# Kernel optimization log

Hardware: AMD Instinct MI355X
Metric: run time of the kernel (lower is better)

Reference implementation:

```python
import jax, jax.numpy as jnp
import numpy as np
import math

N_NODES = 50000
N_EDGES = 1600000
DIM = 64
HEADS = 8
EDGE_DIM = 32


def setup_inputs() -> dict:
    key = jax.random.key(0)
    ks = jax.random.split(key, 12)
    s = 1.0 / math.sqrt(DIM)
    se = 1.0 / math.sqrt(EDGE_DIM)
    return {
        'x': jax.random.normal(ks[0], (N_NODES, DIM), jnp.float32),
        'edge_index': jax.random.randint(ks[1], (2, N_EDGES), 0, N_NODES),
        'edge_attr': jax.random.normal(ks[2], (N_EDGES, EDGE_DIM), jnp.float32),
        'WQ': jax.random.normal(ks[3], (DIM, DIM), jnp.float32) * s,
        'bQ': jnp.zeros((DIM,), jnp.float32),
        'WK': jax.random.normal(ks[4], (DIM, DIM), jnp.float32) * s,
        'bK': jnp.zeros((DIM,), jnp.float32),
        'WV': jax.random.normal(ks[5], (DIM, DIM), jnp.float32) * s,
        'bV': jnp.zeros((DIM,), jnp.float32),
        'WO': jax.random.normal(ks[6], (DIM, DIM), jnp.float32) * s,
        'bO': jnp.zeros((DIM,), jnp.float32),
        'We1': jax.random.normal(ks[7], (EDGE_DIM, EDGE_DIM), jnp.float32) * se,
        'be1': jnp.zeros((EDGE_DIM,), jnp.float32),
        'We2': jax.random.normal(ks[8], (EDGE_DIM, HEADS), jnp.float32) * se,
        'be2': jnp.zeros((HEADS,), jnp.float32),
    }


def graph_softmax(src, index, num_segments):
    # src: [E, H], index: [E] -> per-destination-node stable softmax
    smax = jax.ops.segment_max(src, index, num_segments=num_segments)  # [N, H]
    smax = jnp.where(jnp.isfinite(smax), smax, 0.0)  # nodes with no edges
    e = jnp.exp(src - smax[index])
    ssum = jax.ops.segment_sum(e, index, num_segments=num_segments) + 1e-12
    return e / ssum[index]


def reference(x, edge_index, edge_attr, WQ, bQ, WK, bK, WV, bV, WO, bO, We1, be1, We2, be2):
    num_nodes = x.shape[0]
    d_k = DIM // HEADS
    i, j = edge_index[0], edge_index[1]
    # per-node projections [N, H, d_k], then gather per-edge
    Q = (x @ WQ + bQ).reshape(num_nodes, HEADS, d_k)
    K = (x @ WK + bK).reshape(num_nodes, HEADS, d_k)
    V = (x @ WV + bV).reshape(num_nodes, HEADS, d_k)
    query = Q[j]  # [E, H, d_k]
    key = K[i]
    value = V[i]
    # edge bias MLP: [edge_dim -> edge_dim -> num_heads] with SiLU between
    h = jax.nn.silu(edge_attr @ We1 + be1)
    bias = h @ We2 + be2  # [E, H]
    scores = jnp.sum(query * key, axis=-1) / math.sqrt(d_k) + bias  # [E, H]
    alpha = graph_softmax(scores, j, num_nodes)  # [E, H]
    weighted = (alpha[..., None] * value).reshape(-1, DIM)  # [E, dim]
    attn_out = jax.ops.segment_sum(weighted, j, num_segments=num_nodes)  # [N, dim]
    return attn_out @ WO + bO
```

## Files before the change

### kernel.cpp

```cpp
#include <hip/hip_runtime.h>
#include <math.h>

#define N_NODES 50000
#define N_EDGES 1600000
#define DIM 64
#define HEADS 8
#define EDGE_DIM 32

#define NB 256
#define NPB 196
#define ACAP 8192
#define PART_T 512
#define EPT 4
#define PART_E (PART_T * EPT)

typedef __fp16 h2 __attribute__((ext_vector_type(2)));

__device__ __forceinline__ unsigned int f2bf(float f) {
    union { float f; unsigned int u; } c; c.f = f;
    unsigned int u = c.u;
    return (u + 0x7FFFu + ((u >> 16) & 1u)) >> 16;
}
__device__ __forceinline__ float bf_lo(unsigned int u) { return __uint_as_float(u << 16); }
__device__ __forceinline__ float bf_hi(unsigned int u) { return __uint_as_float(u & 0xFFFF0000u); }

__global__ __launch_bounds__(1024) void pack_weights(
    const float* __restrict__ We1, const float* __restrict__ We2,
    h2* __restrict__ w1p, h2* __restrict__ w2p)
{
    const int t = threadIdx.x;
    if (t < 512) {
        const int c = t >> 4, kk = t & 15;
        w1p[t] = __builtin_amdgcn_cvt_pkrtz(We1[(2 * kk) * EDGE_DIM + c],
                                            We1[(2 * kk + 1) * EDGE_DIM + c]);
    } else if (t < 512 + 128) {
        const int u = t - 512;
        const int h = u >> 4, cc = u & 15;
        w2p[u] = __builtin_amdgcn_cvt_pkrtz(We2[(2 * cc) * HEADS + h],
                                            We2[(2 * cc + 1) * HEADS + h]);
    }
}

__global__ __launch_bounds__(512) void mlp_partition(
    const int* __restrict__ ei,
    const float* __restrict__ edge_attr,
    const h2* __restrict__ w1p, const float* __restrict__ be1,
    const h2* __restrict__ w2p, const float* __restrict__ be2,
    int* __restrict__ gcur,
    unsigned int* __restrict__ A_rec, uint4* __restrict__ A_bias)
{
    __shared__ int cnt[NB];
    __shared__ int base[NB];
    __shared__ int lbase[NB];
    __shared__ int total_s;
    __shared__ unsigned int srec[PART_E];
    __shared__ uint4 sbias[PART_E];
    __shared__ unsigned char sbkt[PART_E];
    const int tid = threadIdx.x;
    if (tid < NB) cnt[tid] = 0;
    __syncthreads();
    const int e0 = blockIdx.x * PART_E;
    #pragma unroll
    for (int k = 0; k < EPT; ++k) {
        const int e = e0 + k * PART_T + tid;
        if (e < N_EDGES) atomicAdd(&cnt[ei[N_EDGES + e] / NPB], 1);
    }
    __syncthreads();
    if (tid < NB) lbase[tid] = cnt[tid];
    __syncthreads();
    for (int o = 1; o < NB; o <<= 1) {
        int t = 0;
        if (tid < NB && tid >= o) t = lbase[tid - o];
        __syncthreads();
        if (tid < NB) lbase[tid] += t;
        __syncthreads();
    }
    if (tid < NB) {
        const int inc = lbase[tid];
        const int c = cnt[tid];
        base[tid] = (c > 0) ? atomicAdd(&gcur[tid], c) : 0;
        lbase[tid] = inc - c;
        if (tid == NB - 1) total_s = inc;
        cnt[tid] = 0;
    }
    __syncthreads();
    for (int k = 0; k < EPT; ++k) {
        const int e = e0 + k * PART_T + tid;
        if (e >= N_EDGES) break;
        const int i = ei[e];
        const int j = ei[N_EDGES + e];
        const int b = j / NPB;
        const int jl = j - b * NPB;
        float a[EDGE_DIM];
        const float4* ar = (const float4*)(edge_attr + (size_t)e * EDGE_DIM);
        #pragma unroll
        for (int q = 0; q < EDGE_DIM / 4; ++q) {
            float4 v = ar[q];
            a[q * 4 + 0] = v.x; a[q * 4 + 1] = v.y;
            a[q * 4 + 2] = v.z; a[q * 4 + 3] = v.w;
        }
        h2 a2[EDGE_DIM / 2];
        #pragma unroll
        for (int kk = 0; kk < EDGE_DIM / 2; ++kk)
            a2[kk] = __builtin_amdgcn_cvt_pkrtz(a[2 * kk], a[2 * kk + 1]);
        float sil[EDGE_DIM];
        #pragma unroll 8
        for (int c = 0; c < EDGE_DIM; ++c) {
            float s = be1[c];
            #pragma unroll
            for (int kk = 0; kk < EDGE_DIM / 2; ++kk)
                s = __builtin_amdgcn_fdot2(a2[kk], w1p[c * 16 + kk], s, false);
            sil[c] = __fdividef(s, 1.0f + __expf(-s));
        }
        h2 s2[EDGE_DIM / 2];
        #pragma unroll
        for (int cc = 0; cc < EDGE_DIM / 2; ++cc)
            s2[cc] = __builtin_amdgcn_cvt_pkrtz(sil[2 * cc], sil[2 * cc + 1]);
        float b0f = be2[0], b1f = be2[1], b2f = be2[2], b3f = be2[3];
        float b4f = be2[4], b5f = be2[5], b6f = be2[6], b7f = be2[7];
        #pragma unroll
        for (int cc = 0; cc < EDGE_DIM / 2; ++cc) {
            b0f = __builtin_amdgcn_fdot2(s2[cc], w2p[0 * 16 + cc], b0f, false);
            b1f = __builtin_amdgcn_fdot2(s2[cc], w2p[1 * 16 + cc], b1f, false);
            b2f = __builtin_amdgcn_fdot2(s2[cc], w2p[2 * 16 + cc], b2f, false);
            b3f = __builtin_amdgcn_fdot2(s2[cc], w2p[3 * 16 + cc], b3f, false);
            b4f = __builtin_amdgcn_fdot2(s2[cc], w2p[4 * 16 + cc], b4f, false);
            b5f = __builtin_amdgcn_fdot2(s2[cc], w2p[5 * 16 + cc], b5f, false);
            b6f = __builtin_amdgcn_fdot2(s2[cc], w2p[6 * 16 + cc], b6f, false);
            b7f = __builtin_amdgcn_fdot2(s2[cc], w2p[7 * 16 + cc], b7f, false);
        }
        uint4 br;
        br.x = f2bf(b0f) | (f2bf(b1f) << 16);
        br.y = f2bf(b2f) | (f2bf(b3f) << 16);
        br.z = f2bf(b4f) | (f2bf(b5f) << 16);
        br.w = f2bf(b6f) | (f2bf(b7f) << 16);
        const int s = lbase[b] + atomicAdd(&cnt[b], 1);
        srec[s] = ((unsigned)jl << 24) | (unsigned)i;
        sbias[s] = br;
        sbkt[s] = (unsigned char)b;
    }
    __syncthreads();
    const int total = total_s;
    for (int s = tid; s < total; s += PART_T) {
        const int b = sbkt[s];
        const int gp = base[b] + (s - lbase[b]);
        if (gp < ACAP) {
            A_rec[(size_t)b * ACAP + gp]  = srec[s];
            A_bias[(size_t)b * ACAP + gp] = sbias[s];
        }
    }
}

__global__ __launch_bounds__(512) void bucket_perm(
    const int* __restrict__ gcur,
    const unsigned int* __restrict__ A_rec,
    int* __restrict__ offs, int* __restrict__ src_sorted, int* __restrict__ perm)
{
    __shared__ int sc[NB];
    __shared__ int ldeg[NPB];
    __shared__ int loff[NPB + 1];
    __shared__ int gbase_s;
    const int tid = threadIdx.x;
    const int b = blockIdx.x;
    if (tid < NB) sc[tid] = min(gcur[tid], ACAP);
    __syncthreads();
    for (int o = 1; o < NB; o <<= 1) {
        int t = 0;
        if (tid < NB && tid >= o) t = sc[tid - o];
        __syncthreads();
        if (tid < NB) sc[tid] += t;
        __syncthreads();
    }
    if (tid == 0) gbase_s = (b == 0) ? 0 : sc[b - 1];
    if (tid < NPB) ldeg[tid] = 0;
    __syncthreads();
    const int gbase = gbase_s;
    const int nb = min(gcur[b], ACAP);
    for (int r = tid; r < nb; r += 512)
        atomicAdd(&ldeg[A_rec[(size_t)b * ACAP + r] >> 24], 1);
    __syncthreads();
    if (tid < 256) sc[tid] = (tid < NPB) ? ldeg[tid] : 0;
    __syncthreads();
    for (int o = 1; o < 256; o <<= 1) {
        int t = 0;
        if (tid < 256 && tid >= o) t = sc[tid - o];
        __syncthreads();
        if (tid < 256) sc[tid] += t;
        __syncthreads();
    }
    if (tid == 0) loff[0] = 0;
    if (tid < NPB) { loff[tid + 1] = sc[tid]; ldeg[tid] = 0; }
    __syncthreads();
    const int jbase = b * NPB;
    if (tid < NPB && jbase + tid < N_NODES) offs[jbase + tid] = gbase + loff[tid];
    if (b == NB - 1 && tid == 0) offs[N_NODES] = gbase + nb;
    for (int r = tid; r < nb; r += 512) {
        const unsigned int rec = A_rec[(size_t)b * ACAP + r];
        const int jl = rec >> 24;
        const int slot = loff[jl] + atomicAdd(&ldeg[jl], 1);
        const int gp = gbase + slot;
        src_sorted[gp] = (int)(rec & 0xFFFFFFu);
        perm[gp] = b * ACAP + r;
    }
}

__global__ __launch_bounds__(256) void qkv_proj(
    const float* __restrict__ x,
    const float* __restrict__ WQ, const float* __restrict__ bQ,
    const float* __restrict__ WK, const float* __restrict__ bK,
    const float* __restrict__ WV, const float* __restrict__ bV,
    float* __restrict__ Q, unsigned int* __restrict__ KV)
{
    __shared__ float sWQ[DIM * DIM];
    __shared__ float sWK[DIM * DIM];
    __shared__ float sWV[DIM * DIM];
    for (int t = threadIdx.x; t < DIM * DIM; t += blockDim.x) {
        sWQ[t] = WQ[t]; sWK[t] = WK[t]; sWV[t] = WV[t];
    }
    __syncthreads();
    const int lane = threadIdx.x & 63;
    const int wave = threadIdx.x >> 6;
    const int n = blockIdx.x * 4 + wave;
    if (n >= N_NODES) return;
    float xl = x[(size_t)n * DIM + lane];
    float aq = bQ[lane], ak = bK[lane], av = bV[lane];
    #pragma unroll
    for (int k = 0; k < DIM; ++k) {
        float xv = __shfl(xl, k, 64);
        aq += xv * sWQ[k * DIM + lane];
        ak += xv * sWK[k * DIM + lane];
        av += xv * sWV[k * DIM + lane];
    }
    Q[(size_t)n * DIM + lane] = aq;
    KV[(size_t)n * DIM + lane] = f2bf(ak) | (f2bf(av) << 16);
}

__global__ __launch_bounds__(256) void node_attn_out(
    const int* __restrict__ off,
    const int* __restrict__ src_sorted,
    const int* __restrict__ perm,
    const unsigned short* __restrict__ bias_u16,
    const float* __restrict__ Q, const unsigned int* __restrict__ KV,
    const float* __restrict__ WO, const float* __restrict__ bO,
    float* __restrict__ out)
{
    __shared__ float sWO[DIM * DIM];
    for (int t = threadIdx.x; t < DIM * DIM; t += 256) sWO[t] = WO[t];
    __syncthreads();
    const int lane = threadIdx.x & 63;
    const int wave = threadIdx.x >> 6;
    const int j = blockIdx.x * 4 + wave;
    if (j >= N_NODES) return;
    const int beg = off[j], end = off[j + 1];
    const int h = lane >> 3;
    const float qv = Q[(size_t)j * DIM + lane];
    const float inv_sqrt_dk = 0.35355339059327373f;
    float num = 0.0f;
    float den = 1e-12f;
    int t = beg;
    for (; t + 3 < end; t += 4) {
        const int i0 = src_sorted[t + 0];
        const int i1 = src_sorted[t + 1];
        const int i2 = src_sorted[t + 2];
        const int i3 = src_sorted[t + 3];
        const int p0 = perm[t + 0];
        const int p1 = perm[t + 1];
        const int p2 = perm[t + 2];
        const int p3 = perm[t + 3];
        const unsigned int u0 = KV[(size_t)i0 * DIM + lane];
        const unsigned int u1 = KV[(size_t)i1 * DIM + lane];
        const unsigned int u2 = KV[(size_t)i2 * DIM + lane];
        const unsigned int u3 = KV[(size_t)i3 * DIM + lane];
        const float b0 = bf_lo((unsigned int)bias_u16[(size_t)p0 * HEADS + h]);
        const float b1 = bf_lo((unsigned int)bias_u16[(size_t)p1 * HEADS + h]);
        const float b2 = bf_lo((unsigned int)bias_u16[(size_t)p2 * HEADS + h]);
        const float b3 = bf_lo((unsigned int)bias_u16[(size_t)p3 * HEADS + h]);
        float d0 = qv * bf_lo(u0);
        float d1 = qv * bf_lo(u1);
        float d2 = qv * bf_lo(u2);
        float d3 = qv * bf_lo(u3);
        d0 += __shfl_xor(d0, 1, 64); d1 += __shfl_xor(d1, 1, 64);
        d2 += __shfl_xor(d2, 1, 64); d3 += __shfl_xor(d3, 1, 64);
        d0 += __shfl_xor(d0, 2, 64); d1 += __shfl_xor(d1, 2, 64);
        d2 += __shfl_xor(d2, 2, 64); d3 += __shfl_xor(d3, 2, 64);
        d0 += __shfl_xor(d0, 4, 64); d1 += __shfl_xor(d1, 4, 64);
        d2 += __shfl_xor(d2, 4, 64); d3 += __shfl_xor(d3, 4, 64);
        const float e0 = __expf(d0 * inv_sqrt_dk + b0);
        const float e1 = __expf(d1 * inv_sqrt_dk + b1);
        const float e2 = __expf(d2 * inv_sqrt_dk + b2);
        const float e3 = __expf(d3 * inv_sqrt_dk + b3);
        num += e0 * bf_hi(u0) + e1 * bf_hi(u1) + e2 * bf_hi(u2) + e3 * bf_hi(u3);
        den += e0 + e1 + e2 + e3;
    }
    for (; t < end; ++t) {
        const int i0 = src_sorted[t];
        const unsigned int u0 = KV[(size_t)i0 * DIM + lane];
        const float b0 = bf_lo((unsigned int)bias_u16[(size_t)perm[t] * HEADS + h]);
        float d0 = qv * bf_lo(u0);
        d0 += __shfl_xor(d0, 1, 64);
        d0 += __shfl_xor(d0, 2, 64);
        d0 += __shfl_xor(d0, 4, 64);
        const float e0 = __expf(d0 * inv_sqrt_dk + b0);
        num += e0 * bf_hi(u0);
        den += e0;
    }
    const float av = num / den;
    float acc = bO[lane];
    #pragma unroll
    for (int k = 0; k < DIM; ++k) {
        acc += __shfl(av, k, 64) * sWO[k * DIM + lane];
    }
    out[(size_t)j * DIM + lane] = acc;
}

extern "C" void kernel_launch(void* const* d_in, const int* in_sizes, int n_in,
                              void* d_out, int out_size, void* d_ws, size_t ws_size,
                              hipStream_t stream) {
    const float* x    = (const float*)d_in[0];
    const int*   ei   = (const int*)d_in[1];
    const float* ea   = (const float*)d_in[2];
    const float* WQ   = (const float*)d_in[3];
    const float* bQ   = (const float*)d_in[4];
    const float* WK   = (const float*)d_in[5];
    const float* bK   = (const float*)d_in[6];
    const float* WV   = (const float*)d_in[7];
    const float* bV   = (const float*)d_in[8];
    const float* WO   = (const float*)d_in[9];
    const float* bO   = (const float*)d_in[10];
    const float* We1  = (const float*)d_in[11];
    const float* be1  = (const float*)d_in[12];
    const float* We2  = (const float*)d_in[13];
    const float* be2  = (const float*)d_in[14];
    float* out = (float*)d_out;

    char* ws = (char*)d_ws;
    size_t off_b = 0;
    auto alloc = [&](size_t bytes) {
        void* p = ws + off_b;
        off_b += (bytes + 255) & ~(size_t)255;
        return p;
    };
    float*        Q          = (float*)alloc((size_t)N_NODES * DIM * sizeof(float));
    unsigned int* KV         = (unsigned int*)alloc((size_t)N_NODES * DIM * sizeof(unsigned int));
    unsigned int* A_rec      = (unsigned int*)alloc((size_t)NB * ACAP * sizeof(unsigned int));
    uint4*        A_bias     = (uint4*)alloc((size_t)NB * ACAP * sizeof(uint4));
    int*          src_sorted = (int*)alloc((size_t)N_EDGES * sizeof(int));
    int*          perm       = (int*)alloc((size_t)N_EDGES * sizeof(int));
    int*          offs       = (int*)alloc((size_t)(N_NODES + 1) * sizeof(int));
    int*          gcur       = (int*)alloc((size_t)NB * sizeof(int));
    h2*           w1p        = (h2*)alloc(512 * sizeof(h2));
    h2*           w2p        = (h2*)alloc(128 * sizeof(h2));

    (void)hipMemsetAsync(gcur, 0, (size_t)NB * sizeof(int), stream);

    pack_weights<<<1, 1024, 0, stream>>>(We1, We2, w1p, w2p);
    mlp_partition<<<(N_EDGES + PART_E - 1) / PART_E, PART_T, 0, stream>>>(
        ei, ea, w1p, be1, w2p, be2, gcur, A_rec, A_bias);
    bucket_perm<<<NB, 512, 0, stream>>>(gcur, A_rec, offs, src_sorted, perm);
    qkv_proj<<<(N_NODES + 3) / 4, 256, 0, stream>>>(x, WQ, bQ, WK, bK, WV, bV, Q, KV);
    node_attn_out<<<(N_NODES + 3) / 4, 256, 0, stream>>>(offs, src_sorted, perm,
                                                         (const unsigned short*)A_bias,
                                                         Q, KV, WO, bO, out);
}
```

Before: 349.8 us.

## Fuse edge-bias MLP and per-node sorting into the attention kernel

The edge MLP moves out of the partition kernel into a new fused attention kernel, and the separate bucket_perm pass is dropped. Each of 8 blocks per bucket rescans the bucket's records, counting-sorts its 25 destination nodes in LDS, computes the edge biases into shared memory, then runs the per-node softmax aggregation and output projection. This removes the global write and read of per-edge biases and the src_sorted/perm arrays, plus one launch. In exchange, every sub-block rereads the whole bucket, edge_attr is gathered in random order rather than streamed, WO is read from global memory rather than LDS, and edges beyond CAPQ per sub-bucket would be silently dropped.

```diff
diff --git a/kernel.cpp b/kernel.cpp
--- a/kernel.cpp
+++ b/kernel.cpp
@@ -10,8 +10,12 @@
 #define NB 256
 #define NPB 196
 #define ACAP 8192
+#define QS 8
+#define NQ 25
+#define CAPQ 1280
+
 #define PART_T 512
-#define EPT 4
+#define EPT 8
 #define PART_E (PART_T * EPT)
 
 typedef __fp16 h2 __attribute__((ext_vector_type(2)));
@@ -41,20 +45,14 @@
     }
 }
 
-__global__ __launch_bounds__(512) void mlp_partition(
-    const int* __restrict__ ei,
-    const float* __restrict__ edge_attr,
-    const h2* __restrict__ w1p, const float* __restrict__ be1,
-    const h2* __restrict__ w2p, const float* __restrict__ be2,
-    int* __restrict__ gcur,
-    unsigned int* __restrict__ A_rec, uint4* __restrict__ A_bias)
+__global__ __launch_bounds__(512) void partition(
+    const int* __restrict__ ei, int* __restrict__ gcur, uint2* __restrict__ A_rec)
 {
     __shared__ int cnt[NB];
     __shared__ int base[NB];
     __shared__ int lbase[NB];
     __shared__ int total_s;
-    __shared__ unsigned int srec[PART_E];
-    __shared__ uint4 sbias[PART_E];
+    __shared__ uint2 srec[PART_E];
     __shared__ unsigned char sbkt[PART_E];
     const int tid = threadIdx.x;
     if (tid < NB) cnt[tid] = 0;
@@ -84,123 +82,25 @@
         cnt[tid] = 0;
     }
     __syncthreads();
+    #pragma unroll
     for (int k = 0; k < EPT; ++k) {
         const int e = e0 + k * PART_T + tid;
-        if (e >= N_EDGES) break;
-        const int i = ei[e];
-        const int j = ei[N_EDGES + e];
-        const int b = j / NPB;
-        const int jl = j - b * NPB;
-        float a[EDGE_DIM];
-        const float4* ar = (const float4*)(edge_attr + (size_t)e * EDGE_DIM);
-        #pragma unroll
-        for (int q = 0; q < EDGE_DIM / 4; ++q) {
-            float4 v = ar[q];
-            a[q * 4 + 0] = v.x; a[q * 4 + 1] = v.y;
-            a[q * 4 + 2] = v.z; a[q * 4 + 3] = v.w;
-        }
-        h2 a2[EDGE_DIM / 2];
-        #pragma unroll
-        for (int kk = 0; kk < EDGE_DIM / 2; ++kk)
-            a2[kk] = __builtin_amdgcn_cvt_pkrtz(a[2 * kk], a[2 * kk + 1]);
-        float sil[EDGE_DIM];
-        #pragma unroll 8
-        for (int c = 0; c < EDGE_DIM; ++c) {
-            float s = be1[c];
-            #pragma unroll
-            for (int kk = 0; kk < EDGE_DIM / 2; ++kk)
-                s = __builtin_amdgcn_fdot2(a2[kk], w1p[c * 16 + kk], s, false);
-            sil[c] = __fdividef(s, 1.0f + __expf(-s));
-        }
-        h2 s2[EDGE_DIM / 2];
-        #pragma unroll
-        for (int cc = 0; cc < EDGE_DIM / 2; ++cc)
-            s2[cc] = __builtin_amdgcn_cvt_pkrtz(sil[2 * cc], sil[2 * cc + 1]);
-        float b0f = be2[0], b1f = be2[1], b2f = be2[2], b3f = be2[3];
-        float b4f = be2[4], b5f = be2[5], b6f = be2[6], b7f = be2[7];
-        #pragma unroll
-        for (int cc = 0; cc < EDGE_DIM / 2; ++cc) {
-            b0f = __builtin_amdgcn_fdot2(s2[cc], w2p[0 * 16 + cc], b0f, false);
-            b1f = __builtin_amdgcn_fdot2(s2[cc], w2p[1 * 16 + cc], b1f, false);
-            b2f = __builtin_amdgcn_fdot2(s2[cc], w2p[2 * 16 + cc], b2f, false);
-            b3f = __builtin_amdgcn_fdot2(s2[cc], w2p[3 * 16 + cc], b3f, false);
-            b4f = __builtin_amdgcn_fdot2(s2[cc], w2p[4 * 16 + cc], b4f, false);
-            b5f = __builtin_amdgcn_fdot2(s2[cc], w2p[5 * 16 + cc], b5f, false);
-            b6f = __builtin_amdgcn_fdot2(s2[cc], w2p[6 * 16 + cc], b6f, false);
-            b7f = __builtin_amdgcn_fdot2(s2[cc], w2p[7 * 16 + cc], b7f, false);
-        }
-        uint4 br;
-        br.x = f2bf(b0f) | (f2bf(b1f) << 16);
-        br.y = f2bf(b2f) | (f2bf(b3f) << 16);
-        br.z = f2bf(b4f) | (f2bf(b5f) << 16);
-        br.w = f2bf(b6f) | (f2bf(b7f) << 16);
-        const int s = lbase[b] + atomicAdd(&cnt[b], 1);
-        srec[s] = ((unsigned)jl << 24) | (unsigned)i;
-        sbias[s] = br;
-        sbkt[s] = (unsigned char)b;
+        if (e < N_EDGES) {
+            const int i = ei[e];
+            const int j = ei[N_EDGES + e];
+            const int b = j / NPB;
+            const int jl = j - b * NPB;
+            const int s = lbase[b] + atomicAdd(&cnt[b], 1);
+            srec[s] = make_uint2((unsigned)e, ((unsigned)jl << 24) | (unsigned)i);
+            sbkt[s] = (unsigned char)b;
+        }
     }
     __syncthreads();
     const int total = total_s;
     for (int s = tid; s < total; s += PART_T) {
         const int b = sbkt[s];
         const int gp = base[b] + (s - lbase[b]);
-        if (gp < ACAP) {
-            A_rec[(size_t)b * ACAP + gp]  = srec[s];
-            A_bias[(size_t)b * ACAP + gp] = sbias[s];
-        }
-    }
-}
-
-__global__ __launch_bounds__(512) void bucket_perm(
-    const int* __restrict__ gcur,
-    const unsigned int* __restrict__ A_rec,
-    int* __restrict__ offs, int* __restrict__ src_sorted, int* __restrict__ perm)
-{
-    __shared__ int sc[NB];
-    __shared__ int ldeg[NPB];
-    __shared__ int loff[NPB + 1];
-    __shared__ int gbase_s;
-    const int tid = threadIdx.x;
-    const int b = blockIdx.x;
-    if (tid < NB) sc[tid] = min(gcur[tid], ACAP);
-    __syncthreads();
-    for (int o = 1; o < NB; o <<= 1) {
-        int t = 0;
-        if (tid < NB && tid >= o) t = sc[tid - o];
-        __syncthreads();
-        if (tid < NB) sc[tid] += t;
-        __syncthreads();
-    }
-    if (tid == 0) gbase_s = (b == 0) ? 0 : sc[b - 1];
-    if (tid < NPB) ldeg[tid] = 0;
-    __syncthreads();
-    const int gbase = gbase_s;
-    const int nb = min(gcur[b], ACAP);
-    for (int r = tid; r < nb; r += 512)
-        atomicAdd(&ldeg[A_rec[(size_t)b * ACAP + r] >> 24], 1);
-    __syncthreads();
-    if (tid < 256) sc[tid] = (tid < NPB) ? ldeg[tid] : 0;
-    __syncthreads();
-    for (int o = 1; o < 256; o <<= 1) {
-        int t = 0;
-        if (tid < 256 && tid >= o) t = sc[tid - o];
-        __syncthreads();
-        if (tid < 256) sc[tid] += t;
-        __syncthreads();
-    }
-    if (tid == 0) loff[0] = 0;
-    if (tid < NPB) { loff[tid + 1] = sc[tid]; ldeg[tid] = 0; }
-    __syncthreads();
-    const int jbase = b * NPB;
-    if (tid < NPB && jbase + tid < N_NODES) offs[jbase + tid] = gbase + loff[tid];
-    if (b == NB - 1 && tid == 0) offs[N_NODES] = gbase + nb;
-    for (int r = tid; r < nb; r += 512) {
-        const unsigned int rec = A_rec[(size_t)b * ACAP + r];
-        const int jl = rec >> 24;
-        const int slot = loff[jl] + atomicAdd(&ldeg[jl], 1);
-        const int gp = gbase + slot;
-        src_sorted[gp] = (int)(rec & 0xFFFFFFu);
-        perm[gp] = b * ACAP + r;
+        if (gp < ACAP) A_rec[(size_t)b * ACAP + gp] = srec[s];
     }
 }
 
@@ -235,82 +135,170 @@
     KV[(size_t)n * DIM + lane] = f2bf(ak) | (f2bf(av) << 16);
 }
 
-__global__ __launch_bounds__(256) void node_attn_out(
-    const int* __restrict__ off,
-    const int* __restrict__ src_sorted,
-    const int* __restrict__ perm,
-    const unsigned short* __restrict__ bias_u16,
+__global__ __launch_bounds__(256) void attn_fused(
+    const int* __restrict__ gcur, const uint2* __restrict__ A_rec,
+    const float* __restrict__ edge_attr,
+    const h2* __restrict__ w1p, const float* __restrict__ be1,
+    const h2* __restrict__ w2p, const float* __restrict__ be2,
     const float* __restrict__ Q, const unsigned int* __restrict__ KV,
     const float* __restrict__ WO, const float* __restrict__ bO,
     float* __restrict__ out)
 {
-    __shared__ float sWO[DIM * DIM];
-    for (int t = threadIdx.x; t < DIM * DIM; t += 256) sWO[t] = WO[t];
-    __syncthreads();
-    const int lane = threadIdx.x & 63;
-    const int wave = threadIdx.x >> 6;
-    const int j = blockIdx.x * 4 + wave;
-    if (j >= N_NODES) return;
-    const int beg = off[j], end = off[j + 1];
+    __shared__ unsigned int lds_e[CAPQ];
+    __shared__ unsigned short lds_i[CAPQ];
+    __shared__ uint4 sbias[CAPQ];
+    __shared__ int loff[NQ + 1];
+    __shared__ int lcur[NQ];
+    __shared__ int ldeg[NQ];
+    const int tid = threadIdx.x;
+    const int bq = blockIdx.x;
+    const int b = bq >> 3;
+    const int q = bq & 7;
+    const int jl0 = q * NQ;
+    const int jl1 = (jl0 + NQ < NPB) ? jl0 + NQ : NPB;
+    const int nqn = jl1 - jl0;
+    const int nb = min(gcur[b], ACAP);
+    if (tid < NQ) ldeg[tid] = 0;
+    __syncthreads();
+    for (int r = tid; r < nb; r += 256) {
+        const int jl = (int)(A_rec[(size_t)b * ACAP + r].y >> 24);
+        if (jl >= jl0 && jl < jl1) atomicAdd(&ldeg[jl - jl0], 1);
+    }
+    __syncthreads();
+    if (tid < 64) {
+        int v = (tid < nqn) ? ldeg[tid] : 0;
+        #pragma unroll
+        for (int o = 1; o < 32; o <<= 1) {
+            int t = __shfl_up(v, o, 64);
+            if (tid >= o) v += t;
+        }
+        if (tid == 0) loff[0] = 0;
+        if (tid < nqn) { loff[tid + 1] = v; lcur[tid] = 0; }
+    }
+    __syncthreads();
+    for (int r = tid; r < nb; r += 256) {
+        const uint2 rec = A_rec[(size_t)b * ACAP + r];
+        const int jl = (int)(rec.y >> 24);
+        if (jl >= jl0 && jl < jl1) {
+            const int s = loff[jl - jl0] + atomicAdd(&lcur[jl - jl0], 1);
+            if (s < CAPQ) {
+                lds_e[s] = rec.x;
+                lds_i[s] = (unsigned short)(rec.y & 0xFFFFFFu);
+            }
+        }
+    }
+    __syncthreads();
+    const int tot = (loff[nqn] < CAPQ) ? loff[nqn] : CAPQ;
+    for (int s = tid; s < tot; s += 256) {
+        const int e = (int)lds_e[s];
+        float a[EDGE_DIM];
+        const float4* ar = (const float4*)(edge_attr + (size_t)e * EDGE_DIM);
+        #pragma unroll
+        for (int p = 0; p < EDGE_DIM / 4; ++p) {
+            float4 v = ar[p];
+            a[p * 4 + 0] = v.x; a[p * 4 + 1] = v.y;
+            a[p * 4 + 2] = v.z; a[p * 4 + 3] = v.w;
+        }
+        h2 a2[EDGE_DIM / 2];
+        #pragma unroll
+        for (int kk = 0; kk < EDGE_DIM / 2; ++kk)
+            a2[kk] = __builtin_amdgcn_cvt_pkrtz(a[2 * kk], a[2 * kk + 1]);
+        float sil[EDGE_DIM];
+        #pragma unroll 8
+        for (int c = 0; c < EDGE_DIM; ++c) {
+            float sv = be1[c];
+            #pragma unroll
+            for (int kk = 0; kk < EDGE_DIM / 2; ++kk)
+                sv = __builtin_amdgcn_fdot2(a2[kk], w1p[c * 16 + kk], sv, false);
+            sil[c] = __fdividef(sv, 1.0f + __expf(-sv));
+        }
+        h2 s2[EDGE_DIM / 2];
+        #pragma unroll
+        for (int cc = 0; cc < EDGE_DIM / 2; ++cc)
+            s2[cc] = __builtin_amdgcn_cvt_pkrtz(sil[2 * cc], sil[2 * cc + 1]);
+        float b0f = be2[0], b1f = be2[1], b2f = be2[2], b3f = be2[3];
+        float b4f = be2[4], b5f = be2[5], b6f = be2[6], b7f = be2[7];
+        #pragma unroll
+        for (int cc = 0; cc < EDGE_DIM / 2; ++cc) {
+            b0f = __builtin_amdgcn_fdot2(s2[cc], w2p[0 * 16 + cc], b0f, false);
+            b1f = __builtin_amdgcn_fdot2(s2[cc], w2p[1 * 16 + cc], b1f, false);
+            b2f = __builtin_amdgcn_fdot2(s2[cc], w2p[2 * 16 + cc], b2f, false);
+            b3f = __builtin_amdgcn_fdot2(s2[cc], w2p[3 * 16 + cc], b3f, false);
+            b4f = __builtin_amdgcn_fdot2(s2[cc], w2p[4 * 16 + cc], b4f, false);
+            b5f = __builtin_amdgcn_fdot2(s2[cc], w2p[5 * 16 + cc], b5f, false);
+            b6f = __builtin_amdgcn_fdot2(s2[cc], w2p[6 * 16 + cc], b6f, false);
+            b7f = __builtin_amdgcn_fdot2(s2[cc], w2p[7 * 16 + cc], b7f, false);
+        }
+        uint4 br;
+        br.x = f2bf(b0f) | (f2bf(b1f) << 16);
+        br.y = f2bf(b2f) | (f2bf(b3f) << 16);
+        br.z = f2bf(b4f) | (f2bf(b5f) << 16);
+        br.w = f2bf(b6f) | (f2bf(b7f) << 16);
+        sbias[s] = br;
+    }
+    __syncthreads();
+    const int lane = tid & 63;
+    const int wave = tid >> 6;
     const int h = lane >> 3;
-    const float qv = Q[(size_t)j * DIM + lane];
+    const unsigned short* sb16 = (const unsigned short*)sbias;
     const float inv_sqrt_dk = 0.35355339059327373f;
-    float num = 0.0f;
-    float den = 1e-12f;
-    int t = beg;
-    for (; t + 3 < end; t += 4) {
-        const int i0 = src_sorted[t + 0];
-        const int i1 = src_sorted[t + 1];
-        const int i2 = src_sorted[t + 2];
-        const int i3 = src_sorted[t + 3];
-        const int p0 = perm[t + 0];
-        const int p1 = perm[t + 1];
-        const int p2 = perm[t + 2];
-        const int p3 = perm[t + 3];
-        const unsigned int u0 = KV[(size_t)i0 * DIM + lane];
-        const unsigned int u1 = KV[(size_t)i1 * DIM + lane];
-        const unsigned int u2 = KV[(size_t)i2 * DIM + lane];
-        const unsigned int u3 = KV[(size_t)i3 * DIM + lane];
-        const float b0 = bf_lo((unsigned int)bias_u16[(size_t)p0 * HEADS + h]);
-        const float b1 = bf_lo((unsigned int)bias_u16[(size_t)p1 * HEADS + h]);
-        const float b2 = bf_lo((unsigned int)bias_u16[(size_t)p2 * HEADS + h]);
-        const float b3 = bf_lo((unsigned int)bias_u16[(size_t)p3 * HEADS + h]);
-        float d0 = qv * bf_lo(u0);
-        float d1 = qv * bf_lo(u1);
-        float d2 = qv * bf_lo(u2);
-        float d3 = qv * bf_lo(u3);
-        d0 += __shfl_xor(d0, 1, 64); d1 += __shfl_xor(d1, 1, 64);
-        d2 += __shfl_xor(d2, 1, 64); d3 += __shfl_xor(d3, 1, 64);
-        d0 += __shfl_xor(d0, 2, 64); d1 += __shfl_xor(d1, 2, 64);
-        d2 += __shfl_xor(d2, 2, 64); d3 += __shfl_xor(d3, 2, 64);
-        d0 += __shfl_xor(d0, 4, 64); d1 += __shfl_xor(d1, 4, 64);
-        d2 += __shfl_xor(d2, 4, 64); d3 += __shfl_xor(d3, 4, 64);
-        const float e0 = __expf(d0 * inv_sqrt_dk + b0);
-        const float e1 = __expf(d1 * inv_sqrt_dk + b1);
-        const float e2 = __expf(d2 * inv_sqrt_dk + b2);
-        const float e3 = __expf(d3 * inv_sqrt_dk + b3);
-        num += e0 * bf_hi(u0) + e1 * bf_hi(u1) + e2 * bf_hi(u2) + e3 * bf_hi(u3);
-        den += e0 + e1 + e2 + e3;
-    }
-    for (; t < end; ++t) {
-        const int i0 = src_sorted[t];
-        const unsigned int u0 = KV[(size_t)i0 * DIM + lane];
-        const float b0 = bf_lo((unsigned int)bias_u16[(size_t)perm[t] * HEADS + h]);
-        float d0 = qv * bf_lo(u0);
-        d0 += __shfl_xor(d0, 1, 64);
-        d0 += __shfl_xor(d0, 2, 64);
-        d0 += __shfl_xor(d0, 4, 64);
-        const float e0 = __expf(d0 * inv_sqrt_dk + b0);
-        num += e0 * bf_hi(u0);
-        den += e0;
-    }
-    const float av = num / den;
-    float acc = bO[lane];
-    #pragma unroll
-    for (int k = 0; k < DIM; ++k) {
-        acc += __shfl(av, k, 64) * sWO[k * DIM + lane];
-    }
-    out[(size_t)j * DIM + lane] = acc;
+    for (int n = wave; n < nqn; n += 4) {
+        const int j = b * NPB + jl0 + n;
+        if (j >= N_NODES) continue;
+        const int beg = (loff[n] < tot) ? loff[n] : tot;
+        const int end = (loff[n + 1] < tot) ? loff[n + 1] : tot;
+        const float qv = Q[(size_t)j * DIM + lane];
+        float num = 0.0f, den = 1e-12f;
+        int t = beg;
+        for (; t + 3 < end; t += 4) {
+            const int i0 = lds_i[t + 0];
+            const int i1 = lds_i[t + 1];
+            const int i2 = lds_i[t + 2];
+            const int i3 = lds_i[t + 3];
+            const unsigned int u0 = KV[(size_t)i0 * DIM + lane];
+            const unsigned int u1 = KV[(size_t)i1 * DIM + lane];
+            const unsigned int u2 = KV[(size_t)i2 * DIM + lane];
+            const unsigned int u3 = KV[(size_t)i3 * DIM + lane];
+            const float b0 = bf_lo((unsigned int)sb16[(t + 0) * 8 + h]);
+            const float b1 = bf_lo((unsigned int)sb16[(t + 1) * 8 + h]);
+            const float b2 = bf_lo((unsigned int)sb16[(t + 2) * 8 + h]);
+            const float b3 = bf_lo((unsigned int)sb16[(t + 3) * 8 + h]);
+            float d0 = qv * bf_lo(u0);
+            float d1 = qv * bf_lo(u1);
+            float d2 = qv * bf_lo(u2);
+            float d3 = qv * bf_lo(u3);
+            d0 += __shfl_xor(d0, 1, 64); d1 += __shfl_xor(d1, 1, 64);
+            d2 += __shfl_xor(d2, 1, 64); d3 += __shfl_xor(d3, 1, 64);
+            d0 += __shfl_xor(d0, 2, 64); d1 += __shfl_xor(d1, 2, 64);
+            d2 += __shfl_xor(d2, 2, 64); d3 += __shfl_xor(d3, 2, 64);
+            d0 += __shfl_xor(d0, 4, 64); d1 += __shfl_xor(d1, 4, 64);
+            d2 += __shfl_xor(d2, 4, 64); d3 += __shfl_xor(d3, 4, 64);
+            const float e0 = __expf(d0 * inv_sqrt_dk + b0);
+            const float e1 = __expf(d1 * inv_sqrt_dk + b1);
+            const float e2 = __expf(d2 * inv_sqrt_dk + b2);
+            const float e3 = __expf(d3 * inv_sqrt_dk + b3);
+            num += e0 * bf_hi(u0) + e1 * bf_hi(u1) + e2 * bf_hi(u2) + e3 * bf_hi(u3);
+            den += e0 + e1 + e2 + e3;
+        }
+        for (; t < end; ++t) {
+            const int i0 = lds_i[t];
+            const unsigned int u0 = KV[(size_t)i0 * DIM + lane];
+            const float b0 = bf_lo((unsigned int)sb16[t * 8 + h]);
+            float d0 = qv * bf_lo(u0);
+            d0 += __shfl_xor(d0, 1, 64);
+            d0 += __shfl_xor(d0, 2, 64);
+            d0 += __shfl_xor(d0, 4, 64);
+            const float e0 = __expf(d0 * inv_sqrt_dk + b0);
+            num += e0 * bf_hi(u0);
+            den += e0;
+        }
+        const float av = num / den;
+        float acc = bO[lane];
+        #pragma unroll
+        for (int k = 0; k < DIM; ++k)
+            acc += __shfl(av, k, 64) * WO[k * DIM + lane];
+        out[(size_t)j * DIM + lane] = acc;
+    }
 }
 
 extern "C" void kernel_launch(void* const* d_in, const int* in_sizes, int n_in,
@@ -340,25 +328,18 @@
         off_b += (bytes + 255) & ~(size_t)255;
         return p;
     };
-    float*        Q          = (float*)alloc((size_t)N_NODES * DIM * sizeof(float));
-    unsigned int* KV         = (unsigned int*)alloc((size_t)N_NODES * DIM * sizeof(unsigned int));
-    unsigned int* A_rec      = (unsigned int*)alloc((size_t)NB * ACAP * sizeof(unsigned int));
-    uint4*        A_bias     = (uint4*)alloc((size_t)NB * ACAP * sizeof(uint4));
-    int*          src_sorted = (int*)alloc((size_t)N_EDGES * sizeof(int));
-    int*          perm       = (int*)alloc((size_t)N_EDGES * sizeof(int));
-    int*          offs       = (int*)alloc((size_t)(N_NODES + 1) * sizeof(int));
-    int*          gcur       = (int*)alloc((size_t)NB * sizeof(int));
-    h2*           w1p        = (h2*)alloc(512 * sizeof(h2));
-    h2*           w2p        = (h2*)alloc(128 * sizeof(h2));
+    float*        Q     = (float*)alloc((size_t)N_NODES * DIM * sizeof(float));
+    unsigned int* KV    = (unsigned int*)alloc((size_t)N_NODES * DIM * sizeof(unsigned int));
+    uint2*        A_rec = (uint2*)alloc((size_t)NB * ACAP * sizeof(uint2));
+    int*          gcur  = (int*)alloc((size_t)NB * sizeof(int));
+    h2*           w1p   = (h2*)alloc(512 * sizeof(h2));
+    h2*           w2p   = (h2*)alloc(128 * sizeof(h2));
 
     (void)hipMemsetAsync(gcur, 0, (size_t)NB * sizeof(int), stream);
 
     pack_weights<<<1, 1024, 0, stream>>>(We1, We2, w1p, w2p);
-    mlp_partition<<<(N_EDGES + PART_E - 1) / PART_E, PART_T, 0, stream>>>(
-        ei, ea, w1p, be1, w2p, be2, gcur, A_rec, A_bias);
-    bucket_perm<<<NB, 512, 0, stream>>>(gcur, A_rec, offs, src_sorted, perm);
+    partition<<<(N_EDGES + PART_E - 1) / PART_E, PART_T, 0, stream>>>(ei, gcur, A_rec);
     qkv_proj<<<(N_NODES + 3) / 4, 256, 0, stream>>>(x, WQ, bQ, WK, bK, WV, bV, Q, KV);
-    node_attn_out<<<(N_NODES + 3) / 4, 256, 0, stream>>>(offs, src_sorted, perm,
-                                                         (const unsigned short*)A_bias,
-                                                         Q, KV, WO, bO, out);
-}
+    attn_fused<<<NB * QS, 256, 0, stream>>>(gcur, A_rec, ea, w1p, be1, w2p, be2,
+                                            Q, KV, WO, bO, out);
+}
```

Measured after the change: 555.3 us. 1.59x slower.
